# Optimization experiments

Hardware: AMD Instinct MI355X
Metric: run time of the kernel (lower is better)

## Reference

```python
import jax, jax.numpy as jnp
import numpy as np

N, F_IN, C, H, L = 4096, 768, 256, 4, 2
DH = C // H  # 64 per-head dim for GATv2


def _ln(x, g, b, eps=1e-5):
    mu = x.mean(-1, keepdims=True)
    var = ((x - mu) ** 2).mean(-1, keepdims=True)
    return (x - mu) / jnp.sqrt(var + eps) * g + b


def _gat_layer(x, wl, wr, att, b, src, dst):
    # GATv2Conv: e_ij = att . leaky_relu(Wl x_j + Wr x_i); softmax over incoming j; concat heads.
    xs = (x @ wl).reshape(N, H, DH)  # source transform
    xd = (x @ wr).reshape(N, H, DH)  # target transform
    e = jnp.einsum('ehd,hd->eh', jax.nn.leaky_relu(xs[src] + xd[dst], 0.2), att)  # [E,H]
    m = jax.ops.segment_max(e, dst, num_segments=N)          # segment softmax (stable)
    p = jnp.exp(e - m[dst])
    s = jax.ops.segment_sum(p, dst, num_segments=N)
    alpha = p / (s[dst] + 1e-16)                             # [E,H]
    out = jax.ops.segment_sum(alpha[:, :, None] * xs[src], dst, num_segments=N)
    return out.reshape(N, C) + b


def _mha(x, wq, wk, wv, bq, bk, bv, wo, bo):
    # nn.MultiheadAttention, batch=1 sequence of all news nodes, eval mode.
    q = (x @ wq + bq).reshape(N, H, DH)
    k = (x @ wk + bk).reshape(N, H, DH)
    v = (x @ wv + bv).reshape(N, H, DH)
    scale = np.float32(1.0 / np.sqrt(DH))
    a = jax.nn.softmax(jnp.einsum('nhd,mhd->hnm', q, k) * scale, axis=-1)  # [H,N,N]
    o = jnp.einsum('hnm,mhd->nhd', a, v).reshape(N, C)
    return o @ wo + bo


def setup_inputs() -> dict:
    key = jax.random.key(0)
    ks = jax.random.split(key, 32)
    rn = lambda k, shp: (jax.random.normal(k, shp, dtype=jnp.float32) * 0.02)
    inp = {
        'x': jax.random.normal(ks[0], (N, F_IN), dtype=jnp.float32),
        'edge_index': jax.random.randint(ks[1], (2, N * 64), 0, N, dtype=jnp.int64),
        'emb_w': rn(ks[2], (F_IN, C)), 'emb_b': jnp.zeros((C,), jnp.float32),
        'g1_wl': rn(ks[3], (C, C)), 'g1_wr': rn(ks[4], (C, C)),
        'g1_att': rn(ks[5], (H, DH)), 'g1_b': jnp.zeros((C,), jnp.float32),
        'g2_wl': rn(ks[6], (C, C)), 'g2_wr': rn(ks[7], (C, C)),
        'g2_att': rn(ks[8], (H, DH)), 'g2_b': jnp.zeros((C,), jnp.float32),
        'mha_wq': rn(ks[9], (C, C)), 'mha_wk': rn(ks[10], (C, C)), 'mha_wv': rn(ks[11], (C, C)),
        'mha_bq': jnp.zeros((C,), jnp.float32), 'mha_bk': jnp.zeros((C,), jnp.float32),
        'mha_bv': jnp.zeros((C,), jnp.float32),
        'mha_wo': rn(ks[12], (C, C)), 'mha_bo': jnp.zeros((C,), jnp.float32),
        'ln_g': jnp.ones((C,), jnp.float32), 'ln_b': jnp.zeros((C,), jnp.float32),
        'cls_w1': rn(ks[13], (C, C // 2)), 'cls_b1': jnp.zeros((C // 2,), jnp.float32),
        'cls_w2': rn(ks[14], (C // 2, 2)), 'cls_b2': jnp.zeros((2,), jnp.float32),
    }
    return inp


def reference(x, edge_index, emb_w, emb_b, g1_wl, g1_wr, g1_att, g1_b,
              g2_wl, g2_wr, g2_att, g2_b, mha_wq, mha_wk, mha_wv, mha_bq,
              mha_bk, mha_bv, mha_wo, mha_bo, ln_g, ln_b,
              cls_w1, cls_b1, cls_w2, cls_b2):
    # add self loops (GATv2Conv default add_self_loops=True)
    loops = jnp.arange(N, dtype=edge_index.dtype)
    src = jnp.concatenate([edge_index[0], loops])
    dst = jnp.concatenate([edge_index[1], loops])

    h = x @ emb_w + emb_b                              # node embedding Linear(-1, C)
    h = jax.nn.relu(_gat_layer(h, g1_wl, g1_wr, g1_att, g1_b, src, dst))
    h = jax.nn.relu(_gat_layer(h, g2_wl, g2_wr, g2_att, g2_b, src, dst))

    # entity-aware self-attention + residual LayerNorm
    enh = _mha(h, mha_wq, mha_wk, mha_wv, mha_bq, mha_bk, mha_bv, mha_wo, mha_bo)
    h = _ln(h + enh, ln_g, ln_b)

    # classifier MLP (dropout = identity in eval)
    h = jax.nn.relu(h @ cls_w1 + cls_b1)
    return h @ cls_w2 + cls_b2
```

## Files before the change

### kernel.cpp

```cpp
#include <hip/hip_runtime.h>

typedef __attribute__((ext_vector_type(8))) short short8_t;
typedef __attribute__((ext_vector_type(4))) float f32x4_t;

#define N_NODES  4096
#define E0_EDGES 262144
#define E_TOTAL  266240
#define SPLITS   8
#define KV_PER_SPLIT (N_NODES / SPLITS)

__device__ __forceinline__ float bf2f(unsigned short u){
  union { unsigned int i; float f; } v; v.i = ((unsigned int)u) << 16; return v.f;
}
__device__ __forceinline__ unsigned short f2bf(float f){
  union { float f; unsigned int i; } v; v.f = f;
  unsigned int r = (v.i + 0x7FFFu + ((v.i >> 16) & 1u)) >> 16;
  return (unsigned short)r;
}
__device__ __forceinline__ unsigned int cvtpk_bf16(float lo, float hi){
  unsigned int r;
  asm volatile("v_cvt_pk_bf16_f32 %0, %1, %2" : "=v"(r) : "v"(lo), "v"(hi));
  return r;
}
template<int CTRL>
__device__ __forceinline__ float dpp_add(float x){
  int v = __builtin_amdgcn_update_dpp(0, __float_as_int(x), CTRL, 0xF, 0xF, true);
  return x + __int_as_float(v);
}
__device__ __forceinline__ float rowsum16(float x){
  x = dpp_add<0xB1>(x); x = dpp_add<0x4E>(x); x = dpp_add<0x124>(x); x = dpp_add<0x128>(x);
  return x;
}
__device__ __forceinline__ void wg_barrier(){
  asm volatile("s_waitcnt lgkmcnt(0)" ::: "memory");
  __builtin_amdgcn_s_barrier();
  asm volatile("" ::: "memory");
}

struct TJob { const float* src; unsigned short* dst; int rows, cols, tile0; };
struct TJobs { TJob j[10]; };

__global__ __launch_bounds__(256) void prep_kernel(const float* __restrict__ x, unsigned short* __restrict__ xb,
                                                   TJobs jobs, int tb, int* __restrict__ zp){
  __shared__ unsigned short tile[64 * 64];
  int b = blockIdx.x, t = threadIdx.x;
  if (b < 3072){
    int i = (b * 256 + t) * 4;
    float4 v = *(const float4*)&x[i];
    union { unsigned short u[4]; uint2 q; } o;
    o.u[0] = f2bf(v.x); o.u[1] = f2bf(v.y); o.u[2] = f2bf(v.z); o.u[3] = f2bf(v.w);
    *(uint2*)&xb[i] = o.q;
    return;
  }
  if (b < 3072 + tb){
    int bb = b - 3072;
    int ji = 0;
    #pragma unroll
    for (int k = 1; k < 10; k++) if (bb >= jobs.j[k].tile0) ji = k;
    TJob J = jobs.j[ji];
    int lt = bb - J.tile0;
    int tpr = J.cols >> 6;
    int tr = lt / tpr, tc = lt - tr * tpr;
    #pragma unroll
    for (int i2 = 0; i2 < 2; i2++){
      int e = i2 * 2048 + t * 8;
      int nl = e >> 6, c8 = e & 63;
      const float* sp = &J.src[(size_t)(tr * 64 + nl) * J.cols + tc * 64 + c8];
      float4 v0 = *(const float4*)sp;
      float4 v1 = *(const float4*)(sp + 4);
      union { unsigned short u[8]; uint4 q; } o;
      o.u[0]=f2bf(v0.x); o.u[1]=f2bf(v0.y); o.u[2]=f2bf(v0.z); o.u[3]=f2bf(v0.w);
      o.u[4]=f2bf(v1.x); o.u[5]=f2bf(v1.y); o.u[6]=f2bf(v1.z); o.u[7]=f2bf(v1.w);
      *(uint4*)&tile[nl * 64 + (((c8 >> 3) ^ ((nl >> 3) & 7)) * 8)] = o.q;
    }
    __syncthreads();
    #pragma unroll
    for (int i2 = 0; i2 < 2; i2++){
      int e = i2 * 2048 + t * 8;
      int cl = e >> 6, n8 = e & 63;
      union { unsigned short u[8]; uint4 q; } o;
      #pragma unroll
      for (int j = 0; j < 8; j++){
        int row = n8 + j;
        o.u[j] = tile[row * 64 + (((cl >> 3) ^ ((row >> 3) & 7)) * 8) + (cl & 7)];
      }
      *(uint4*)&J.dst[(size_t)(tc * 64 + cl) * J.rows + tr * 64 + n8] = o.q;
    }
    return;
  }
  int i = (b - 3072 - tb) * 256 + t;
  if (i < 8192) zp[i] = 0;
}

__global__ __launch_bounds__(256) void scatter_kernel(const int* __restrict__ ei, const int* __restrict__ offs,
                                                      int* __restrict__ cur, int* __restrict__ csrc){
  int e = blockIdx.x * 256 + threadIdx.x;
  if (e >= E_TOTAL) return;
  int s, d;
  if (e < E0_EDGES){ s = ei[e]; d = ei[E0_EDGES + e]; }
  else { s = d = e - E0_EDGES; }
  int pos = offs[d] + atomicAdd(&cur[d], 1);
  csrc[pos] = s;
}

struct GJob { const unsigned short* Wt; const float* bias; float* outF; unsigned short* outB; unsigned short* outT; float scale; };
struct GJobs { GJob j[3]; };
struct AuxJob { int mode; const int* ei; int* a; int* b; };

__global__ __launch_bounds__(256) void gemm_kernel(const unsigned short* __restrict__ A, GJobs jobs,
                                                   int K, int Nc, int relu, AuxJob AX){
  __shared__ unsigned short lds[8192];
  const int t = threadIdx.x;

  if (AX.mode && blockIdx.z == gridDim.z - 1){
    int flat = blockIdx.x + (blockIdx.y << 6);
    if (AX.mode == 1){
      for (int e = flat * 256 + t; e < E_TOTAL; e += 65536){
        int d = (e < E0_EDGES) ? AX.ei[E0_EDGES + e] : (e - E0_EDGES);
        atomicAdd(&AX.a[d], 1);
      }
    } else if (flat == 0){
      int* wtot = (int*)lds;
      int lane = t & 63, w = t >> 6;
      int v[16];
      int base = t * 16;
      int s = 0;
      #pragma unroll
      for (int j = 0; j < 16; j++){ v[j] = AX.a[base + j]; s += v[j]; }
      int x = s;
      #pragma unroll
      for (int off = 1; off < 64; off <<= 1){
        int y = __shfl_up(x, off, 64);
        if (lane >= off) x += y;
      }
      if (lane == 63) wtot[w] = x;
      __syncthreads();
      int wbase = 0;
      #pragma unroll
      for (int k = 0; k < 4; k++) if (k < w) wbase += wtot[k];
      int run = wbase + x - s;
      #pragma unroll
      for (int j = 0; j < 16; j++){ AX.b[base + j] = run; run += v[j]; }
      if (t == 255) AX.b[N_NODES] = run;
    }
    return;
  }

  const GJob job = jobs.j[blockIdx.z];
  const int lane = t & 63, w = t >> 6;
  const int wm = w >> 1, wn = w & 1;
  const int c16 = lane & 15, g = lane >> 4;
  const int bm = blockIdx.x, bn = blockIdx.y;

  const int srow = t >> 2, schunk = t & 3;
  const unsigned short* Ag = A      + (size_t)(bm * 64 + srow) * K + schunk * 8;
  const unsigned short* Bg = job.Wt + (size_t)(bn * 64 + srow) * K + schunk * 8;
  const int swz = srow * 32 + ((schunk ^ ((srow >> 1) & 3)) * 8);

  const int arow0 = wm * 32 + c16, arow1 = arow0 + 16;
  const int aoff0 = arow0 * 32 + ((g ^ ((arow0 >> 1) & 3)) * 8);
  const int aoff1 = arow1 * 32 + ((g ^ ((arow1 >> 1) & 3)) * 8);
  const int bcol0 = wn * 32 + c16, bcol1 = bcol0 + 16;
  const int boff0 = 2048 + bcol0 * 32 + ((g ^ ((bcol0 >> 1) & 3)) * 8);
  const int boff1 = 2048 + bcol1 * 32 + ((g ^ ((bcol1 >> 1) & 3)) * 8);

  f32x4_t acc[2][2] = {};
  const int nk = K >> 5;

  {
    uint4 av = *(const uint4*)(Ag);
    uint4 bv = *(const uint4*)(Bg);
    *(uint4*)&lds[swz]        = av;
    *(uint4*)&lds[2048 + swz] = bv;
  }
  int cur = 0;
  for (int i = 0; i < nk; i++){
    const bool pf = (i + 1) < nk;
    uint4 av, bv;
    if (pf){
      av = *(const uint4*)(Ag + (i + 1) * 32);
      bv = *(const uint4*)(Bg + (i + 1) * 32);
    }
    wg_barrier();
    const int base = cur * 4096;
    union { uint4 u; short8_t s; } a0, a1, b0, b1;
    a0.u = *(const uint4*)&lds[base + aoff0];
    a1.u = *(const uint4*)&lds[base + aoff1];
    b0.u = *(const uint4*)&lds[base + boff0];
    b1.u = *(const uint4*)&lds[base + boff1];
    acc[0][0] = __builtin_amdgcn_mfma_f32_16x16x32_bf16(a0.s, b0.s, acc[0][0], 0, 0, 0);
    acc[0][1] = __builtin_amdgcn_mfma_f32_16x16x32_bf16(a0.s, b1.s, acc[0][1], 0, 0, 0);
    acc[1][0] = __builtin_amdgcn_mfma_f32_16x16x32_bf16(a1.s, b0.s, acc[1][0], 0, 0, 0);
    acc[1][1] = __builtin_amdgcn_mfma_f32_16x16x32_bf16(a1.s, b1.s, acc[1][1], 0, 0, 0);
    if (pf){
      const int nb = (cur ^ 1) * 4096;
      *(uint4*)&lds[nb + swz]        = av;
      *(uint4*)&lds[nb + 2048 + swz] = bv;
      cur ^= 1;
    }
  }

  #pragma unroll
  for (int fm = 0; fm < 2; fm++){
    #pragma unroll
    for (int fn = 0; fn < 2; fn++){
      int col = bn * 64 + wn * 32 + fn * 16 + c16;
      float bia = job.bias ? job.bias[col] : 0.f;
      float vv[4];
      #pragma unroll
      for (int r = 0; r < 4; r++){
        float v = (acc[fm][fn][r] + bia) * job.scale;
        if (relu) v = fmaxf(v, 0.f);
        vv[r] = v;
      }
      int row0 = bm * 64 + wm * 32 + fm * 16 + g * 4;
      if (job.outF){
        #pragma unroll
        for (int r = 0; r < 4; r++) job.outF[(size_t)(row0 + r) * Nc + col] = vv[r];
      }
      if (job.outB){
        #pragma unroll
        for (int r = 0; r < 4; r++) job.outB[(size_t)(row0 + r) * Nc + col] = f2bf(vv[r]);
      }
      if (job.outT){
        union { unsigned short u[4]; uint2 q; } pk;
        #pragma unroll
        for (int r = 0; r < 4; r++) pk.u[r] = f2bf(vv[r]);
        *(uint2*)&job.outT[(size_t)col * 4096 + row0] = pk.q;
      }
    }
  }
}

__global__ __launch_bounds__(256) void gat_gather(const unsigned short* __restrict__ xs, const unsigned short* __restrict__ xd,
                                                  const float* __restrict__ att, const float* __restrict__ bias,
                                                  const int* __restrict__ offs, const int* __restrict__ csrc,
                                                  unsigned short* __restrict__ outB, float* __restrict__ outF){
  __shared__ float combL[4][256];
  __shared__ float combS[4][4];
  const int i = blockIdx.x, t = threadIdx.x;
  const int lane = t & 63, w = t >> 6;
  float xdc[4], attc[4];
  {
    uint2 xv = *(const uint2*)&xd[i * 256 + lane * 4];
    xdc[0] = bf2f((unsigned short)(xv.x & 0xffff)); xdc[1] = bf2f((unsigned short)(xv.x >> 16));
    xdc[2] = bf2f((unsigned short)(xv.y & 0xffff)); xdc[3] = bf2f((unsigned short)(xv.y >> 16));
    float4 av = *(const float4*)&att[lane * 4];
    attc[0] = av.x; attc[1] = av.y; attc[2] = av.z; attc[3] = av.w;
  }
  const int b0 = offs[i], b1 = offs[i + 1];
  float acc0 = 0.f, acc1 = 0.f, acc2 = 0.f, acc3 = 0.f, ssum = 0.f;
  int p = b0 + w;
  for (; p + 4 < b1; p += 8){
    int sA = csrc[p], sB = csrc[p + 4];
    uint2 xa = *(const uint2*)&xs[sA * 256 + lane * 4];
    uint2 xb = *(const uint2*)&xs[sB * 256 + lane * 4];
    float a0 = bf2f((unsigned short)(xa.x & 0xffff)), a1 = bf2f((unsigned short)(xa.x >> 16));
    float a2 = bf2f((unsigned short)(xa.y & 0xffff)), a3 = bf2f((unsigned short)(xa.y >> 16));
    float b0_ = bf2f((unsigned short)(xb.x & 0xffff)), b1_ = bf2f((unsigned short)(xb.x >> 16));
    float b2_ = bf2f((unsigned short)(xb.y & 0xffff)), b3_ = bf2f((unsigned short)(xb.y >> 16));
    float va0 = a0 + xdc[0]; va0 = (va0 > 0.f) ? va0 : 0.2f * va0;
    float va1 = a1 + xdc[1]; va1 = (va1 > 0.f) ? va1 : 0.2f * va1;
    float va2 = a2 + xdc[2]; va2 = (va2 > 0.f) ? va2 : 0.2f * va2;
    float va3 = a3 + xdc[3]; va3 = (va3 > 0.f) ? va3 : 0.2f * va3;
    float vb0 = b0_ + xdc[0]; vb0 = (vb0 > 0.f) ? vb0 : 0.2f * vb0;
    float vb1 = b1_ + xdc[1]; vb1 = (vb1 > 0.f) ? vb1 : 0.2f * vb1;
    float vb2 = b2_ + xdc[2]; vb2 = (vb2 > 0.f) ? vb2 : 0.2f * vb2;
    float vb3 = b3_ + xdc[3]; vb3 = (vb3 > 0.f) ? vb3 : 0.2f * vb3;
    float eA = rowsum16(va0 * attc[0] + va1 * attc[1] + va2 * attc[2] + va3 * attc[3]);
    float eB = rowsum16(vb0 * attc[0] + vb1 * attc[1] + vb2 * attc[2] + vb3 * attc[3]);
    float pA = __expf(eA), pB = __expf(eB);
    ssum += pA + pB;
    acc0 += pA * a0 + pB * b0_; acc1 += pA * a1 + pB * b1_;
    acc2 += pA * a2 + pB * b2_; acc3 += pA * a3 + pB * b3_;
  }
  if (p < b1){
    int s = csrc[p];
    uint2 xv = *(const uint2*)&xs[s * 256 + lane * 4];
    float x0 = bf2f((unsigned short)(xv.x & 0xffff)), x1 = bf2f((unsigned short)(xv.x >> 16));
    float x2 = bf2f((unsigned short)(xv.y & 0xffff)), x3 = bf2f((unsigned short)(xv.y >> 16));
    float v0 = x0 + xdc[0]; v0 = (v0 > 0.f) ? v0 : 0.2f * v0;
    float v1 = x1 + xdc[1]; v1 = (v1 > 0.f) ? v1 : 0.2f * v1;
    float v2 = x2 + xdc[2]; v2 = (v2 > 0.f) ? v2 : 0.2f * v2;
    float v3 = x3 + xdc[3]; v3 = (v3 > 0.f) ? v3 : 0.2f * v3;
    float e = rowsum16(v0 * attc[0] + v1 * attc[1] + v2 * attc[2] + v3 * attc[3]);
    float pe = __expf(e);
    ssum += pe;
    acc0 += pe * x0; acc1 += pe * x1; acc2 += pe * x2; acc3 += pe * x3;
  }
  combL[w][lane * 4 + 0] = acc0; combL[w][lane * 4 + 1] = acc1;
  combL[w][lane * 4 + 2] = acc2; combL[w][lane * 4 + 3] = acc3;
  if ((lane & 15) == 0) combS[w][lane >> 4] = ssum;
  __syncthreads();
  float atot = combL[0][t] + combL[1][t] + combL[2][t] + combL[3][t];
  int hh = t >> 6;
  float stot = combS[0][hh] + combS[1][hh] + combS[2][hh] + combS[3][hh];
  float o = atot / (stot + 1e-16f) + bias[t];
  o = fmaxf(o, 0.f);
  outB[i * 256 + t] = f2bf(o);
  if (outF) outF[i * 256 + t] = o;
}

__global__ __launch_bounds__(512, 2) void attn_kernel(const unsigned short* __restrict__ qb, const unsigned short* __restrict__ kb,
                                                      const unsigned short* __restrict__ vt,
                                                      float* __restrict__ Opart, float* __restrict__ Ol){
  __shared__ unsigned short K_lds[2][4096];
  __shared__ unsigned short V_lds[2][4096];
  __shared__ unsigned short P_lds[8][2048];
  const int t = threadIdx.x, lane = t & 63, w = t >> 6;
  const int c16 = lane & 15, g = lane >> 4;
  const int h = blockIdx.y, bq = blockIdx.x, sp = blockIdx.z;

  const int sr = t >> 3, sc = (t & 7) * 8;
  const int kw = sr * 64 + (((t & 7) ^ ((sr >> 1) & 7)) * 8);
  const int vw = sr * 64 + (((t & 7) ^ (sr & 7)) * 8);

  short8_t qa[2][2];
  #pragma unroll
  for (int qm = 0; qm < 2; qm++){
    int qrow = bq * 256 + w * 32 + qm * 16 + c16;
    union { uint4 u; short8_t s; } cv0, cv1;
    cv0.u = *(const uint4*)&qb[(size_t)qrow * 256 + h * 64 + g * 8];
    cv1.u = *(const uint4*)&qb[(size_t)qrow * 256 + h * 64 + 32 + g * 8];
    qa[qm][0] = cv0.s; qa[qm][1] = cv1.s;
  }

  f32x4_t oacc[2][4] = {};
  float lsum[2] = {0.f, 0.f};

  const int kv_lo = sp * KV_PER_SPLIT;
  {
    uint4 k0 = *(const uint4*)&kb[(size_t)(kv_lo + sr) * 256 + h * 64 + sc];
    uint4 v0 = *(const uint4*)&vt[(size_t)(h * 64 + sr) * 4096 + kv_lo + sc];
    *(uint4*)&K_lds[0][kw] = k0;
    *(uint4*)&V_lds[0][vw] = v0;
  }
  int cur = 0;

  for (int ti = 0; ti < KV_PER_SPLIT / 64; ti++){
    const bool pf = (ti + 1) < KV_PER_SPLIT / 64;
    uint4 nk, nv;
    if (pf){
      int kvn = kv_lo + (ti + 1) * 64;
      nk = *(const uint4*)&kb[(size_t)(kvn + sr) * 256 + h * 64 + sc];
      nv = *(const uint4*)&vt[(size_t)(h * 64 + sr) * 4096 + kvn + sc];
    }
    wg_barrier();
    const unsigned short* Kb = K_lds[cur];
    const unsigned short* Vb = V_lds[cur];
    unsigned short* Pw = P_lds[w];

    f32x4_t sacc[2][4] = {};
    #pragma unroll
    for (int kd = 0; kd < 2; kd++){
      #pragma unroll
      for (int fn = 0; fn < 4; fn++){
        union { uint4 u; short8_t s; } kf;
        kf.u = *(const uint4*)&Kb[(fn * 16 + c16) * 64 + (((kd * 4 + g) ^ ((c16 >> 1) & 7)) * 8)];
        sacc[0][fn] = __builtin_amdgcn_mfma_f32_16x16x32_bf16(kf.s, qa[0][kd], sacc[0][fn], 0, 0, 0);
        sacc[1][fn] = __builtin_amdgcn_mfma_f32_16x16x32_bf16(kf.s, qa[1][kd], sacc[1][fn], 0, 0, 0);
      }
    }

    #pragma unroll
    for (int qm = 0; qm < 2; qm++){
      float ps = 0.f;
      int row = qm * 16 + c16;
      #pragma unroll
      for (int fn = 0; fn < 4; fn++){
        float p0 = __expf(sacc[qm][fn][0]);
        float p1 = __expf(sacc[qm][fn][1]);
        float p2 = __expf(sacc[qm][fn][2]);
        float p3 = __expf(sacc[qm][fn][3]);
        ps += (p0 + p1) + (p2 + p3);
        uint2 pk;
        pk.x = cvtpk_bf16(p0, p1);
        pk.y = cvtpk_bf16(p2, p3);
        int chunk = (fn * 2 + (g >> 1)) ^ (c16 & 7);
        *(uint2*)&Pw[row * 64 + chunk * 8 + (g & 1) * 4] = pk;
      }
      ps += __shfl_xor(ps, 16, 64);
      ps += __shfl_xor(ps, 32, 64);
      lsum[qm] += ps;
    }

    #pragma unroll
    for (int kd2 = 0; kd2 < 2; kd2++){
      const int ch = (((kd2 * 4 + g) ^ (c16 & 7)) * 8);
      union { uint4 u; short8_t s; } pt0, pt1;
      pt0.u = *(const uint4*)&Pw[c16 * 64 + ch];
      pt1.u = *(const uint4*)&Pw[(16 + c16) * 64 + ch];
      #pragma unroll
      for (int fn = 0; fn < 4; fn++){
        union { uint4 u; short8_t s; } vf;
        vf.u = *(const uint4*)&Vb[(fn * 16 + c16) * 64 + ch];
        oacc[0][fn] = __builtin_amdgcn_mfma_f32_16x16x32_bf16(vf.s, pt0.s, oacc[0][fn], 0, 0, 0);
        oacc[1][fn] = __builtin_amdgcn_mfma_f32_16x16x32_bf16(vf.s, pt1.s, oacc[1][fn], 0, 0, 0);
      }
    }

    if (pf){
      *(uint4*)&K_lds[cur ^ 1][kw] = nk;
      *(uint4*)&V_lds[cur ^ 1][vw] = nv;
      cur ^= 1;
    }
  }

  const int sh = sp * 4 + h;
  #pragma unroll
  for (int qm = 0; qm < 2; qm++){
    int node = bq * 256 + w * 32 + qm * 16 + c16;
    #pragma unroll
    for (int fn = 0; fn < 4; fn++){
      *(float4*)&Opart[((size_t)sh * N_NODES + node) * 64 + fn * 16 + g * 4] =
        *(float4*)&oacc[qm][fn];
    }
    if (g == 0) Ol[(size_t)sh * N_NODES + node] = lsum[qm];
  }
}

__global__ __launch_bounds__(256) void wo_ln_cls_kernel(const float* __restrict__ Opart, const float* __restrict__ Ol,
                                                        const unsigned short* __restrict__ Wt, const float* __restrict__ bo,
                                                        const float* __restrict__ h2f, const float* __restrict__ gg,
                                                        const float* __restrict__ bb,
                                                        const unsigned short* __restrict__ Wt1, const float* __restrict__ b1,
                                                        const float* __restrict__ w2, const float* __restrict__ b2,
                                                        float* __restrict__ out){
  __shared__ unsigned short Ab[2][512];
  __shared__ unsigned short Bb[2][8192];
  __shared__ unsigned short Cb[2][4096];
  __shared__ unsigned short hl[16 * 264];
  __shared__ float red1[4][16], red2[4][16];
  __shared__ float cred0[4][16], cred1[4][16];
  __shared__ float Ls[64];
  const int t = threadIdx.x, lane = t & 63, w = t >> 6;
  const int c16 = lane & 15, g = lane >> 4;
  const int bm = blockIdx.x;

  const int arow = t >> 2, achk = t & 3;
  const int aswz = arow * 32 + ((achk ^ ((arow >> 1) & 3)) * 8);
  const int bq_ = t >> 2, bchk = t & 3;

  if (t < 64){
    int node = bm * 16 + (t >> 2), h = t & 3;
    float L = 0.f;
    #pragma unroll
    for (int s = 0; s < SPLITS; s++) L += Ol[(size_t)(s * 4 + h) * N_NODES + node];
    Ls[t] = 1.f / L;
  }
  __syncthreads();

  const int afr = c16 * 32 + ((g ^ ((c16 >> 1) & 3)) * 8);
  int bfr[4];
  #pragma unroll
  for (int fn = 0; fn < 4; fn++){
    int col = w * 64 + fn * 16 + c16;
    bfr[fn] = col * 32 + ((g ^ ((col >> 1) & 3)) * 8);
  }

  const int anode = bm * 16 + arow;
  auto loadA = [&](int k0, float4* pa){
    int c0 = k0 + achk * 8;
    int hh = c0 >> 6, d0 = c0 & 63;
    #pragma unroll
    for (int s = 0; s < SPLITS; s++){
      const float* bp = &Opart[((size_t)(s * 4 + hh) * N_NODES + anode) * 64 + d0];
      pa[s * 2]     = *(const float4*)bp;
      pa[s * 2 + 1] = *(const float4*)(bp + 4);
    }
  };
  auto packA = [&](int k0, const float4* pa) -> uint4 {
    float a[8] = {0.f,0.f,0.f,0.f,0.f,0.f,0.f,0.f};
    #pragma unroll
    for (int s = 0; s < SPLITS; s++){
      a[0] += pa[s*2].x;   a[1] += pa[s*2].y;   a[2] += pa[s*2].z;   a[3] += pa[s*2].w;
      a[4] += pa[s*2+1].x; a[5] += pa[s*2+1].y; a[6] += pa[s*2+1].z; a[7] += pa[s*2+1].w;
    }
    int c0 = k0 + achk * 8;
    float Li = Ls[(arow << 2) | (c0 >> 6)];
    union { unsigned short u[8]; uint4 q; } o;
    #pragma unroll
    for (int j = 0; j < 8; j++) o.u[j] = f2bf(a[j] * Li);
    return o.q;
  };

  f32x4_t acc[4] = {};
  {
    if (t < 64){
      float4 pa0[SPLITS * 2];
      loadA(0, pa0);
      *(uint4*)&Ab[0][aswz] = packA(0, pa0);
    }
    #pragma unroll
    for (int j = 0; j < 4; j++){
      int col = j * 64 + bq_;
      *(uint4*)&Bb[0][col * 32 + ((bchk ^ ((col >> 1) & 3)) * 8)] = *(const uint4*)&Wt[(size_t)col * 256 + bchk * 8];
    }
  }
  int cur = 0;
  for (int i = 0; i < 8; i++){
    const bool pf = i < 7;
    float4 pa[SPLITS * 2]; uint4 pb[4];
    int k1 = (i + 1) * 32;
    if (pf){
      if (t < 64) loadA(k1, pa);
      #pragma unroll
      for (int j = 0; j < 4; j++){
        int col = j * 64 + bq_;
        pb[j] = *(const uint4*)&Wt[(size_t)col * 256 + k1 + bchk * 8];
      }
    }
    wg_barrier();
    union { uint4 u; short8_t s; } a, b;
    a.u = *(const uint4*)&Ab[cur][afr];
    #pragma unroll
    for (int fn = 0; fn < 4; fn++){
      b.u = *(const uint4*)&Bb[cur][bfr[fn]];
      acc[fn] = __builtin_amdgcn_mfma_f32_16x16x32_bf16(a.s, b.s, acc[fn], 0, 0, 0);
    }
    if (pf){
      if (t < 64) *(uint4*)&Ab[cur ^ 1][aswz] = packA(k1, pa);
      #pragma unroll
      for (int j = 0; j < 4; j++){
        int col = j * 64 + bq_;
        *(uint4*)&Bb[cur ^ 1][col * 32 + ((bchk ^ ((col >> 1) & 3)) * 8)] = pb[j];
      }
      cur ^= 1;
    }
  }

  float vv[4][4];
  #pragma unroll
  for (int fn = 0; fn < 4; fn++){
    int col = w * 64 + fn * 16 + c16;
    float bia = bo[col];
    #pragma unroll
    for (int r = 0; r < 4; r++)
      vv[fn][r] = acc[fn][r] + bia + h2f[(size_t)(bm * 16 + g * 4 + r) * 256 + col];
  }
  #pragma unroll
  for (int r = 0; r < 4; r++){
    float a = 0.f, b = 0.f;
    #pragma unroll
    for (int fn = 0; fn < 4; fn++){ a += vv[fn][r]; b += vv[fn][r] * vv[fn][r]; }
    a = rowsum16(a); b = rowsum16(b);
    if (c16 == 0){ red1[w][g * 4 + r] = a; red2[w][g * 4 + r] = b; }
  }
  __syncthreads();
  #pragma unroll
  for (int r = 0; r < 4; r++){
    int row = g * 4 + r;
    float S1 = red1[0][row] + red1[1][row] + red1[2][row] + red1[3][row];
    float S2 = red2[0][row] + red2[1][row] + red2[2][row] + red2[3][row];
    float mean = S1 * (1.f / 256.f);
    float var = S2 * (1.f / 256.f) - mean * mean;
    float rs = rsqrtf(var + 1e-5f);
    #pragma unroll
    for (int fn = 0; fn < 4; fn++){
      int col = w * 64 + fn * 16 + c16;
      hl[row * 264 + col] = f2bf((vv[fn][r] - mean) * rs * gg[col] + bb[col]);
    }
  }

  wg_barrier();
  int cfr[2];
  #pragma unroll
  for (int fn = 0; fn < 2; fn++){
    int col = w * 32 + fn * 16 + c16;
    cfr[fn] = col * 32 + ((g ^ ((col >> 1) & 3)) * 8);
  }
  f32x4_t cacc[2] = {};
  {
    #pragma unroll
    for (int j = 0; j < 2; j++){
      int col = j * 64 + bq_;
      *(uint4*)&Cb[0][col * 32 + ((bchk ^ ((col >> 1) & 3)) * 8)] = *(const uint4*)&Wt1[(size_t)col * 256 + bchk * 8];
    }
  }
  cur = 0;
  for (int i = 0; i < 8; i++){
    const bool pf = i < 7;
    uint4 pb[2];
    if (pf){
      int k1 = (i + 1) * 32;
      #pragma unroll
      for (int j = 0; j < 2; j++){
        int col = j * 64 + bq_;
        pb[j] = *(const uint4*)&Wt1[(size_t)col * 256 + k1 + bchk * 8];
      }
    }
    wg_barrier();
    union { uint4 u; short8_t s; } a, b;
    a.u = *(const uint4*)&hl[c16 * 264 + i * 32 + g * 8];
    #pragma unroll
    for (int fn = 0; fn < 2; fn++){
      b.u = *(const uint4*)&Cb[cur][cfr[fn]];
      cacc[fn] = __builtin_amdgcn_mfma_f32_16x16x32_bf16(a.s, b.s, cacc[fn], 0, 0, 0);
    }
    if (pf){
      #pragma unroll
      for (int j = 0; j < 2; j++){
        int col = j * 64 + bq_;
        *(uint4*)&Cb[cur ^ 1][col * 32 + ((bchk ^ ((col >> 1) & 3)) * 8)] = pb[j];
      }
      cur ^= 1;
    }
  }
  float cv[2][4];
  #pragma unroll
  for (int fn = 0; fn < 2; fn++){
    int col = w * 32 + fn * 16 + c16;
    float bia = b1[col];
    #pragma unroll
    for (int r = 0; r < 4; r++) cv[fn][r] = fmaxf(cacc[fn][r] + bia, 0.f);
  }
  float w20 = w2[(w * 32 + c16) * 2],      w21 = w2[(w * 32 + c16) * 2 + 1];
  float w30 = w2[(w * 32 + 16 + c16) * 2], w31 = w2[(w * 32 + 16 + c16) * 2 + 1];
  #pragma unroll
  for (int r = 0; r < 4; r++){
    float a0 = cv[0][r] * w20 + cv[1][r] * w30;
    float a1 = cv[0][r] * w21 + cv[1][r] * w31;
    a0 = rowsum16(a0); a1 = rowsum16(a1);
    if (c16 == 0){ cred0[w][g * 4 + r] = a0; cred1[w][g * 4 + r] = a1; }
  }
  __syncthreads();
  if (t < 16){
    float q0 = cred0[0][t] + cred0[1][t] + cred0[2][t] + cred0[3][t] + b2[0];
    float q1 = cred1[0][t] + cred1[1][t] + cred1[2][t] + cred1[3][t] + b2[1];
    out[(size_t)(bm * 16 + t) * 2]     = q0;
    out[(size_t)(bm * 16 + t) * 2 + 1] = q1;
  }
}

extern "C" void kernel_launch(void* const* d_in, const int* in_sizes, int n_in,
                              void* d_out, int out_size, void* d_ws, size_t ws_size,
                              hipStream_t stream){
  const float* x      = (const float*)d_in[0];
  const int*   ei     = (const int*)d_in[1];
  const float* emb_w  = (const float*)d_in[2];
  const float* emb_b  = (const float*)d_in[3];
  const float* g1_wl  = (const float*)d_in[4];
  const float* g1_wr  = (const float*)d_in[5];
  const float* g1_att = (const float*)d_in[6];
  const float* g1_b   = (const float*)d_in[7];
  const float* g2_wl  = (const float*)d_in[8];
  const float* g2_wr  = (const float*)d_in[9];
  const float* g2_att = (const float*)d_in[10];
  const float* g2_b   = (const float*)d_in[11];
  const float* wq     = (const float*)d_in[12];
  const float* wk     = (const float*)d_in[13];
  const float* wv     = (const float*)d_in[14];
  const float* bq     = (const float*)d_in[15];
  const float* bk     = (const float*)d_in[16];
  const float* bv     = (const float*)d_in[17];
  const float* wo     = (const float*)d_in[18];
  const float* bo     = (const float*)d_in[19];
  const float* ln_g   = (const float*)d_in[20];
  const float* ln_b   = (const float*)d_in[21];
  const float* cls_w1 = (const float*)d_in[22];
  const float* cls_b1 = (const float*)d_in[23];
  const float* cls_w2 = (const float*)d_in[24];
  const float* cls_b2 = (const float*)d_in[25];
  float* out = (float*)d_out;

  char* wsb = (char*)d_ws;
  size_t o = 0;
  auto take = [&](size_t bytes) -> char* {
    char* r = wsb + o; o += (bytes + 255) & ~(size_t)255; return r;
  };
  unsigned short* wt_emb  = (unsigned short*)take(768 * 256 * 2);
  unsigned short* wt_wl1  = (unsigned short*)take(256 * 256 * 2);
  unsigned short* wt_wr1  = (unsigned short*)take(256 * 256 * 2);
  unsigned short* wt_wl2  = (unsigned short*)take(256 * 256 * 2);
  unsigned short* wt_wr2  = (unsigned short*)take(256 * 256 * 2);
  unsigned short* wt_wq   = (unsigned short*)take(256 * 256 * 2);
  unsigned short* wt_wk   = (unsigned short*)take(256 * 256 * 2);
  unsigned short* wt_wv   = (unsigned short*)take(256 * 256 * 2);
  unsigned short* wt_wo   = (unsigned short*)take(256 * 256 * 2);
  unsigned short* wt_cls1 = (unsigned short*)take(256 * 128 * 2);
  unsigned short* x_bf    = (unsigned short*)take((size_t)4096 * 768 * 2);
  unsigned short* h0_bf   = (unsigned short*)take((size_t)4096 * 256 * 2);
  unsigned short* xs1_bf  = (unsigned short*)take((size_t)4096 * 256 * 2);
  unsigned short* xd1_bf  = (unsigned short*)take((size_t)4096 * 256 * 2);
  unsigned short* h1_bf   = (unsigned short*)take((size_t)4096 * 256 * 2);
  unsigned short* xs2_bf  = (unsigned short*)take((size_t)4096 * 256 * 2);
  unsigned short* xd2_bf  = (unsigned short*)take((size_t)4096 * 256 * 2);
  unsigned short* h2_bf   = (unsigned short*)take((size_t)4096 * 256 * 2);
  float*          h2_f    = (float*)take((size_t)4096 * 256 * 4);
  unsigned short* q_bf    = (unsigned short*)take((size_t)4096 * 256 * 2);
  unsigned short* k_bf    = (unsigned short*)take((size_t)4096 * 256 * 2);
  unsigned short* vt_bf   = (unsigned short*)take((size_t)4096 * 256 * 2);
  int* deg  = (int*)take(4096 * 4);
  int* cur  = (int*)take(4096 * 4);
  int* offs = (int*)take(4097 * 4);
  int* csrc = (int*)take((size_t)E_TOTAL * 4);
  float* Opart = (float*)take((size_t)SPLITS * 4 * N_NODES * 64 * 4);
  float* Ol    = (float*)take((size_t)SPLITS * 4 * N_NODES * 4);

  TJobs TJ;
  TJob tj[10] = {
    { emb_w,  wt_emb,  768, 256, 0 },
    { g1_wl,  wt_wl1,  256, 256, 0 },
    { g1_wr,  wt_wr1,  256, 256, 0 },
    { g2_wl,  wt_wl2,  256, 256, 0 },
    { g2_wr,  wt_wr2,  256, 256, 0 },
    { wq,     wt_wq,   256, 256, 0 },
    { wk,     wt_wk,   256, 256, 0 },
    { wv,     wt_wv,   256, 256, 0 },
    { wo,     wt_wo,   256, 256, 0 },
    { cls_w1, wt_cls1, 256, 128, 0 },
  };
  int tb = 0;
  for (int i = 0; i < 10; i++){
    tj[i].tile0 = tb;
    tb += (tj[i].rows >> 6) * (tj[i].cols >> 6);
    TJ.j[i] = tj[i];
  }
  prep_kernel<<<3072 + tb + 32, 256, 0, stream>>>(x, x_bf, TJ, tb, deg);

  GJobs J;
  AuxJob AX0 = { 0, nullptr, nullptr, nullptr };
  J = {}; J.j[0] = { wt_emb, emb_b, nullptr, h0_bf, nullptr, 1.f };
  AuxJob AXh = { 1, ei, deg, nullptr };
  gemm_kernel<<<dim3(64, 4, 2), 256, 0, stream>>>(x_bf, J, 768, 256, 0, AXh);
  J = {}; J.j[0] = { wt_wl1, nullptr, nullptr, xs1_bf, nullptr, 1.f }; J.j[1] = { wt_wr1, nullptr, nullptr, xd1_bf, nullptr, 1.f };
  AuxJob AXs = { 2, nullptr, deg, offs };
  gemm_kernel<<<dim3(64, 4, 3), 256, 0, stream>>>(h0_bf, J, 256, 256, 0, AXs);
  scatter_kernel<<<(E_TOTAL + 255) / 256, 256, 0, stream>>>(ei, offs, cur, csrc);
  gat_gather<<<4096, 256, 0, stream>>>(xs1_bf, xd1_bf, g1_att, g1_b, offs, csrc, h1_bf, nullptr);
  J = {}; J.j[0] = { wt_wl2, nullptr, nullptr, xs2_bf, nullptr, 1.f }; J.j[1] = { wt_wr2, nullptr, nullptr, xd2_bf, nullptr, 1.f };
  gemm_kernel<<<dim3(64, 4, 2), 256, 0, stream>>>(h1_bf, J, 256, 256, 0, AX0);
  gat_gather<<<4096, 256, 0, stream>>>(xs2_bf, xd2_bf, g2_att, g2_b, offs, csrc, h2_bf, h2_f);
  J = {};
  J.j[0] = { wt_wq, bq, nullptr, q_bf, nullptr, 0.125f };
  J.j[1] = { wt_wk, bk, nullptr, k_bf, nullptr, 1.f };
  J.j[2] = { wt_wv, bv, nullptr, nullptr, vt_bf, 1.f };
  gemm_kernel<<<dim3(64, 4, 3), 256, 0, stream>>>(h2_bf, J, 256, 256, 0, AX0);
  attn_kernel<<<dim3(16, 4, SPLITS), 512, 0, stream>>>(q_bf, k_bf, vt_bf, Opart, Ol);
  wo_ln_cls_kernel<<<256, 256, 0, stream>>>(Opart, Ol, wt_wo, bo, h2_f, ln_g, ln_b,
                                            wt_cls1, cls_b1, cls_w2, cls_b2, out);

  (void)in_sizes; (void)n_in; (void)out_size; (void)ws_size;
}
```

Baseline: 162.2 us.

## Fuse x fp32→bf16 conversion into embedding GEMM, fp16 attention partials, exp2 softmax

Removes the separate x-to-bf16 conversion pass from the prep kernel. The embedding GEMM now loads fp32 x directly and converts it while staging to LDS, which removes a 6MB write and a re-read. The split-KV attention partial outputs are stored as fp16 instead of fp32, halving the traffic between the attention and Wo kernels. The softmax now uses exp2 with log2(e) folded into the Q scale. The risk is somewhat lower precision in the partial sums and extra fp32 load bandwidth inside the embedding GEMM.

```diff
diff --git a/kernel.cpp b/kernel.cpp
--- a/kernel.cpp
+++ b/kernel.cpp
@@ -36,29 +36,25 @@
   __builtin_amdgcn_s_barrier();
   asm volatile("" ::: "memory");
 }
+__device__ __forceinline__ uint4 cvt8_f32_to_bf16(float4 f0, float4 f1){
+  union { unsigned short u[8]; uint4 q; } o;
+  o.u[0]=f2bf(f0.x); o.u[1]=f2bf(f0.y); o.u[2]=f2bf(f0.z); o.u[3]=f2bf(f0.w);
+  o.u[4]=f2bf(f1.x); o.u[5]=f2bf(f1.y); o.u[6]=f2bf(f1.z); o.u[7]=f2bf(f1.w);
+  return o.q;
+}
 
 struct TJob { const float* src; unsigned short* dst; int rows, cols, tile0; };
 struct TJobs { TJob j[10]; };
 
-__global__ __launch_bounds__(256) void prep_kernel(const float* __restrict__ x, unsigned short* __restrict__ xb,
-                                                   TJobs jobs, int tb, int* __restrict__ zp){
+__global__ __launch_bounds__(256) void prep_kernel(TJobs jobs, int tb, int* __restrict__ zp){
   __shared__ unsigned short tile[64 * 64];
   int b = blockIdx.x, t = threadIdx.x;
-  if (b < 3072){
-    int i = (b * 256 + t) * 4;
-    float4 v = *(const float4*)&x[i];
-    union { unsigned short u[4]; uint2 q; } o;
-    o.u[0] = f2bf(v.x); o.u[1] = f2bf(v.y); o.u[2] = f2bf(v.z); o.u[3] = f2bf(v.w);
-    *(uint2*)&xb[i] = o.q;
-    return;
-  }
-  if (b < 3072 + tb){
-    int bb = b - 3072;
+  if (b < tb){
     int ji = 0;
     #pragma unroll
-    for (int k = 1; k < 10; k++) if (bb >= jobs.j[k].tile0) ji = k;
+    for (int k = 1; k < 10; k++) if (b >= jobs.j[k].tile0) ji = k;
     TJob J = jobs.j[ji];
-    int lt = bb - J.tile0;
+    int lt = b - J.tile0;
     int tpr = J.cols >> 6;
     int tr = lt / tpr, tc = lt - tr * tpr;
     #pragma unroll
@@ -68,10 +64,7 @@
       const float* sp = &J.src[(size_t)(tr * 64 + nl) * J.cols + tc * 64 + c8];
       float4 v0 = *(const float4*)sp;
       float4 v1 = *(const float4*)(sp + 4);
-      union { unsigned short u[8]; uint4 q; } o;
-      o.u[0]=f2bf(v0.x); o.u[1]=f2bf(v0.y); o.u[2]=f2bf(v0.z); o.u[3]=f2bf(v0.w);
-      o.u[4]=f2bf(v1.x); o.u[5]=f2bf(v1.y); o.u[6]=f2bf(v1.z); o.u[7]=f2bf(v1.w);
-      *(uint4*)&tile[nl * 64 + (((c8 >> 3) ^ ((nl >> 3) & 7)) * 8)] = o.q;
+      *(uint4*)&tile[nl * 64 + (((c8 >> 3) ^ ((nl >> 3) & 7)) * 8)] = cvt8_f32_to_bf16(v0, v1);
     }
     __syncthreads();
     #pragma unroll
@@ -88,7 +81,7 @@
     }
     return;
   }
-  int i = (b - 3072 - tb) * 256 + t;
+  int i = (b - tb) * 256 + t;
   if (i < 8192) zp[i] = 0;
 }
 
@@ -107,8 +100,8 @@
 struct GJobs { GJob j[3]; };
 struct AuxJob { int mode; const int* ei; int* a; int* b; };
 
-__global__ __launch_bounds__(256) void gemm_kernel(const unsigned short* __restrict__ A, GJobs jobs,
-                                                   int K, int Nc, int relu, AuxJob AX){
+__global__ __launch_bounds__(256) void gemm_kernel(const unsigned short* __restrict__ A, const float* __restrict__ Af32,
+                                                   GJobs jobs, int K, int Nc, int relu, AuxJob AX){
   __shared__ unsigned short lds[8192];
   const int t = threadIdx.x;
 
@@ -153,7 +146,8 @@
   const int bm = blockIdx.x, bn = blockIdx.y;
 
   const int srow = t >> 2, schunk = t & 3;
-  const unsigned short* Ag = A      + (size_t)(bm * 64 + srow) * K + schunk * 8;
+  const unsigned short* Ag = Af32 ? nullptr : (A + (size_t)(bm * 64 + srow) * K + schunk * 8);
+  const float* Ag32 = Af32 ? (Af32 + (size_t)(bm * 64 + srow) * K + schunk * 8) : nullptr;
   const unsigned short* Bg = job.Wt + (size_t)(bn * 64 + srow) * K + schunk * 8;
   const int swz = srow * 32 + ((schunk ^ ((srow >> 1) & 3)) * 8);
 
@@ -168,7 +162,14 @@
   const int nk = K >> 5;
 
   {
-    uint4 av = *(const uint4*)(Ag);
+    uint4 av;
+    if (Af32){
+      float4 f0 = *(const float4*)(Ag32);
+      float4 f1 = *(const float4*)(Ag32 + 4);
+      av = cvt8_f32_to_bf16(f0, f1);
+    } else {
+      av = *(const uint4*)(Ag);
+    }
     uint4 bv = *(const uint4*)(Bg);
     *(uint4*)&lds[swz]        = av;
     *(uint4*)&lds[2048 + swz] = bv;
@@ -177,8 +178,14 @@
   for (int i = 0; i < nk; i++){
     const bool pf = (i + 1) < nk;
     uint4 av, bv;
+    float4 af0, af1;
     if (pf){
-      av = *(const uint4*)(Ag + (i + 1) * 32);
+      if (Af32){
+        af0 = *(const float4*)(Ag32 + (i + 1) * 32);
+        af1 = *(const float4*)(Ag32 + (i + 1) * 32 + 4);
+      } else {
+        av = *(const uint4*)(Ag + (i + 1) * 32);
+      }
       bv = *(const uint4*)(Bg + (i + 1) * 32);
     }
     wg_barrier();
@@ -194,6 +201,7 @@
     acc[1][1] = __builtin_amdgcn_mfma_f32_16x16x32_bf16(a1.s, b1.s, acc[1][1], 0, 0, 0);
     if (pf){
       const int nb = (cur ^ 1) * 4096;
+      if (Af32) av = cvt8_f32_to_bf16(af0, af1);
       *(uint4*)&lds[nb + swz]        = av;
       *(uint4*)&lds[nb + 2048 + swz] = bv;
       cur ^= 1;
@@ -303,7 +311,7 @@
 
 __global__ __launch_bounds__(512, 2) void attn_kernel(const unsigned short* __restrict__ qb, const unsigned short* __restrict__ kb,
                                                       const unsigned short* __restrict__ vt,
-                                                      float* __restrict__ Opart, float* __restrict__ Ol){
+                                                      _Float16* __restrict__ Opart, float* __restrict__ Ol){
   __shared__ unsigned short K_lds[2][4096];
   __shared__ unsigned short V_lds[2][4096];
   __shared__ unsigned short P_lds[8][2048];
@@ -368,10 +376,10 @@
       int row = qm * 16 + c16;
       #pragma unroll
       for (int fn = 0; fn < 4; fn++){
-        float p0 = __expf(sacc[qm][fn][0]);
-        float p1 = __expf(sacc[qm][fn][1]);
-        float p2 = __expf(sacc[qm][fn][2]);
-        float p3 = __expf(sacc[qm][fn][3]);
+        float p0 = __builtin_exp2f(sacc[qm][fn][0]);
+        float p1 = __builtin_exp2f(sacc[qm][fn][1]);
+        float p2 = __builtin_exp2f(sacc[qm][fn][2]);
+        float p3 = __builtin_exp2f(sacc[qm][fn][3]);
         ps += (p0 + p1) + (p2 + p3);
         uint2 pk;
         pk.x = cvtpk_bf16(p0, p1);
@@ -412,14 +420,16 @@
     int node = bq * 256 + w * 32 + qm * 16 + c16;
     #pragma unroll
     for (int fn = 0; fn < 4; fn++){
-      *(float4*)&Opart[((size_t)sh * N_NODES + node) * 64 + fn * 16 + g * 4] =
-        *(float4*)&oacc[qm][fn];
+      union { _Float16 h[4]; uint2 q; } pk;
+      #pragma unroll
+      for (int r = 0; r < 4; r++) pk.h[r] = (_Float16)oacc[qm][fn][r];
+      *(uint2*)&Opart[((size_t)sh * N_NODES + node) * 64 + fn * 16 + g * 4] = pk.q;
     }
     if (g == 0) Ol[(size_t)sh * N_NODES + node] = lsum[qm];
   }
 }
 
-__global__ __launch_bounds__(256) void wo_ln_cls_kernel(const float* __restrict__ Opart, const float* __restrict__ Ol,
+__global__ __launch_bounds__(256) void wo_ln_cls_kernel(const _Float16* __restrict__ Opart, const float* __restrict__ Ol,
                                                         const unsigned short* __restrict__ Wt, const float* __restrict__ bo,
                                                         const float* __restrict__ h2f, const float* __restrict__ gg,
                                                         const float* __restrict__ bb,
@@ -459,22 +469,20 @@
   }
 
   const int anode = bm * 16 + arow;
-  auto loadA = [&](int k0, float4* pa){
+  auto loadA = [&](int k0, uint4* pa){
     int c0 = k0 + achk * 8;
     int hh = c0 >> 6, d0 = c0 & 63;
     #pragma unroll
+    for (int s = 0; s < SPLITS; s++)
+      pa[s] = *(const uint4*)&Opart[((size_t)(s * 4 + hh) * N_NODES + anode) * 64 + d0];
+  };
+  auto packA = [&](int k0, const uint4* pa) -> uint4 {
+    float a[8] = {0.f,0.f,0.f,0.f,0.f,0.f,0.f,0.f};
+    #pragma unroll
     for (int s = 0; s < SPLITS; s++){
-      const float* bp = &Opart[((size_t)(s * 4 + hh) * N_NODES + anode) * 64 + d0];
-      pa[s * 2]     = *(const float4*)bp;
-      pa[s * 2 + 1] = *(const float4*)(bp + 4);
-    }
-  };
-  auto packA = [&](int k0, const float4* pa) -> uint4 {
-    float a[8] = {0.f,0.f,0.f,0.f,0.f,0.f,0.f,0.f};
-    #pragma unroll
-    for (int s = 0; s < SPLITS; s++){
-      a[0] += pa[s*2].x;   a[1] += pa[s*2].y;   a[2] += pa[s*2].z;   a[3] += pa[s*2].w;
-      a[4] += pa[s*2+1].x; a[5] += pa[s*2+1].y; a[6] += pa[s*2+1].z; a[7] += pa[s*2+1].w;
+      union { uint4 q; _Float16 h[8]; } u; u.q = pa[s];
+      #pragma unroll
+      for (int j = 0; j < 8; j++) a[j] += (float)u.h[j];
     }
     int c0 = k0 + achk * 8;
     float Li = Ls[(arow << 2) | (c0 >> 6)];
@@ -487,7 +495,7 @@
   f32x4_t acc[4] = {};
   {
     if (t < 64){
-      float4 pa0[SPLITS * 2];
+      uint4 pa0[SPLITS];
       loadA(0, pa0);
       *(uint4*)&Ab[0][aswz] = packA(0, pa0);
     }
@@ -500,7 +508,7 @@
   int cur = 0;
   for (int i = 0; i < 8; i++){
     const bool pf = i < 7;
-    float4 pa[SPLITS * 2]; uint4 pb[4];
+    uint4 pa[SPLITS]; uint4 pb[4];
     int k1 = (i + 1) * 32;
     if (pf){
       if (t < 64) loadA(k1, pa);
@@ -678,7 +686,6 @@
   unsigned short* wt_wv   = (unsigned short*)take(256 * 256 * 2);
   unsigned short* wt_wo   = (unsigned short*)take(256 * 256 * 2);
   unsigned short* wt_cls1 = (unsigned short*)take(256 * 128 * 2);
-  unsigned short* x_bf    = (unsigned short*)take((size_t)4096 * 768 * 2);
   unsigned short* h0_bf   = (unsigned short*)take((size_t)4096 * 256 * 2);
   unsigned short* xs1_bf  = (unsigned short*)take((size_t)4096 * 256 * 2);
   unsigned short* xd1_bf  = (unsigned short*)take((size_t)4096 * 256 * 2);
@@ -694,8 +701,8 @@
   int* cur  = (int*)take(4096 * 4);
   int* offs = (int*)take(4097 * 4);
   int* csrc = (int*)take((size_t)E_TOTAL * 4);
-  float* Opart = (float*)take((size_t)SPLITS * 4 * N_NODES * 64 * 4);
-  float* Ol    = (float*)take((size_t)SPLITS * 4 * N_NODES * 4);
+  _Float16* Opart = (_Float16*)take((size_t)SPLITS * 4 * N_NODES * 64 * 2);
+  float*    Ol    = (float*)take((size_t)SPLITS * 4 * N_NODES * 4);
 
   TJobs TJ;
   TJob tj[10] = {
@@ -716,26 +723,26 @@
     tb += (tj[i].rows >> 6) * (tj[i].cols >> 6);
     TJ.j[i] = tj[i];
   }
-  prep_kernel<<<3072 + tb + 32, 256, 0, stream>>>(x, x_bf, TJ, tb, deg);
+  prep_kernel<<<tb + 32, 256, 0, stream>>>(TJ, tb, deg);
 
   GJobs J;
   AuxJob AX0 = { 0, nullptr, nullptr, nullptr };
   J = {}; J.j[0] = { wt_emb, emb_b, nullptr, h0_bf, nullptr, 1.f };
   AuxJob AXh = { 1, ei, deg, nullptr };
-  gemm_kernel<<<dim3(64, 4, 2), 256, 0, stream>>>(x_bf, J, 768, 256, 0, AXh);
+  gemm_kernel<<<dim3(64, 4, 2), 256, 0, stream>>>(nullptr, x, J, 768, 256, 0, AXh);
   J = {}; J.j[0] = { wt_wl1, nullptr, nullptr, xs1_bf, nullptr, 1.f }; J.j[1] = { wt_wr1, nullptr, nullptr, xd1_bf, nullptr, 1.f };
   AuxJob AXs = { 2, nullptr, deg, offs };
-  gemm_kernel<<<dim3(64, 4, 3), 256, 0, stream>>>(h0_bf, J, 256, 256, 0, AXs);
+  gemm_kernel<<<dim3(64, 4, 3), 256, 0, stream>>>(h0_bf, nullptr, J, 256, 256, 0, AXs);
   scatter_kernel<<<(E_TOTAL + 255) / 256, 256, 0, stream>>>(ei, offs, cur, csrc);
   gat_gather<<<4096, 256, 0, stream>>>(xs1_bf, xd1_bf, g1_att, g1_b, offs, csrc, h1_bf, nullptr);
   J = {}; J.j[0] = { wt_wl2, nullptr, nullptr, xs2_bf, nullptr, 1.f }; J.j[1] = { wt_wr2, nullptr, nullptr, xd2_bf, nullptr, 1.f };
-  gemm_kernel<<<dim3(64, 4, 2), 256, 0, stream>>>(h1_bf, J, 256, 256, 0, AX0);
+  gemm_kernel<<<dim3(64, 4, 2), 256, 0, stream>>>(h1_bf, nullptr, J, 256, 256, 0, AX0);
   gat_gather<<<4096, 256, 0, stream>>>(xs2_bf, xd2_bf, g2_att, g2_b, offs, csrc, h2_bf, h2_f);
   J = {};
-  J.j[0] = { wt_wq, bq, nullptr, q_bf, nullptr, 0.125f };
+  J.j[0] = { wt_wq, bq, nullptr, q_bf, nullptr, 0.125f * 1.44269504f };
   J.j[1] = { wt_wk, bk, nullptr, k_bf, nullptr, 1.f };
   J.j[2] = { wt_wv, bv, nullptr, nullptr, vt_bf, 1.f };
-  gemm_kernel<<<dim3(64, 4, 3), 256, 0, stream>>>(h2_bf, J, 256, 256, 0, AX0);
+  gemm_kernel<<<dim3(64, 4, 3), 256, 0, stream>>>(h2_bf, nullptr, J, 256, 256, 0, AX0);
   attn_kernel<<<dim3(16, 4, SPLITS), 512, 0, stream>>>(q_bf, k_bf, vt_bf, Opart, Ol);
   wo_ln_cls_kernel<<<256, 256, 0, stream>>>(Opart, Ol, wt_wo, bo, h2_f, ln_g, ln_b,
                                             wt_cls1, cls_b1, cls_w2, cls_b2, out);
```

Result: slower. 177.0 us (+9.1%).
